# Kernel tuning notes

Hardware: AMD Instinct MI355X
Metric: run time of the kernel (lower is better)

Reference implementation:

```python
import jax, jax.numpy as jnp
import numpy as np

N = 100_000   # total nodes per graph batch
E = 400_000   # directed edges per graph batch
G = 1024      # number of graphs
F_IN = 90


def _lin_init(key, fan_in, fan_out):
    s = 1.0 / np.sqrt(fan_in)
    kW, kb = jax.random.split(key)
    W = jax.random.uniform(kW, (fan_in, fan_out), jnp.float32, -s, s)
    b = jax.random.uniform(kb, (fan_out,), jnp.float32, -s, s)
    return W, b


def setup_inputs() -> dict:
    key = jax.random.key(0)
    ks = jax.random.split(key, 16)
    batch = (jnp.arange(N, dtype=jnp.int32) * G // N).astype(jnp.int32)
    inp = {
        'x1': jax.random.normal(ks[0], (N, F_IN), jnp.float32),
        'edge_index1': jax.random.randint(ks[1], (2, E), 0, N, jnp.int32),
        'batch1': batch,
        'x2': jax.random.normal(ks[2], (N, F_IN), jnp.float32),
        'edge_index2': jax.random.randint(ks[3], (2, E), 0, N, jnp.int32),
        'batch2': batch,
    }
    W1, b1 = _lin_init(ks[4], 90, 128)
    W2, b2 = _lin_init(ks[5], 128, 256)
    W3, b3 = _lin_init(ks[6], 256, 256)
    W4, b4 = _lin_init(ks[7], 256, 256)
    fc1_W, fc1_b = _lin_init(ks[8], 1024, 512)
    fc2_W, fc2_b = _lin_init(ks[9], 512, 256)
    fc3_W, fc3_b = _lin_init(ks[10], 256, 1)
    inp.update(W1=W1, b1=b1, W2=W2, b2=b2, W3=W3, b3=b3, W4=W4, b4=b4,
               fc1_W=fc1_W, fc1_b=fc1_b, fc2_W=fc2_W, fc2_b=fc2_b,
               fc3_W=fc3_W, fc3_b=fc3_b)
    return inp


def _gcn(x, W, b, src, dst, dinv):
    # GCNConv: D^{-1/2} (A + I) D^{-1/2} X W + b  (self-loops added)
    h = x @ W                                   # [N, F_out]
    norm = dinv[src] * dinv[dst]                # [E]
    agg = jax.ops.segment_sum(h[src] * norm[:, None], dst, num_segments=N)
    agg = agg + h * (dinv * dinv)[:, None]      # self-loop term
    return agg + b


def _drug_encoder(x, edge_index, batch, W1, b1, W2, b2, W3, b3, W4, b4):
    src, dst = edge_index[0], edge_index[1]
    # degree with self-loops (PyG gcn_norm)
    deg = jax.ops.segment_sum(jnp.ones(src.shape[0], x.dtype), dst, num_segments=N) + 1.0
    dinv = jax.lax.rsqrt(deg)
    x = jax.nn.relu(_gcn(x, W1, b1, src, dst, dinv))
    x = jax.nn.relu(_gcn(x, W2, b2, src, dst, dinv))
    x = jax.nn.relu(_gcn(x, W3, b3, src, dst, dinv))
    x = jax.nn.relu(_gcn(x, W4, b4, src, dst, dinv))
    gmax = jax.ops.segment_max(x, batch, num_segments=G)
    cnt = jax.ops.segment_sum(jnp.ones(N, x.dtype), batch, num_segments=G)
    gmean = jax.ops.segment_sum(x, batch, num_segments=G) / cnt[:, None]
    return jnp.concatenate([gmax, gmean], axis=1)   # [G, 512]


def reference(x1, edge_index1, batch1, x2, edge_index2, batch2,
              W1, b1, W2, b2, W3, b3, W4, b4,
              fc1_W, fc1_b, fc2_W, fc2_b, fc3_W, fc3_b):
    h1 = _drug_encoder(x1, edge_index1, batch1, W1, b1, W2, b2, W3, b3, W4, b4)
    h2 = _drug_encoder(x2, edge_index2, batch2, W1, b1, W2, b2, W3, b3, W4, b4)
    x = jnp.concatenate([h1 - h2, h2 - h1], axis=1)   # [G, 1024]
    x = jax.nn.relu(x @ fc1_W + fc1_b)                # dropout = identity (eval)
    x = jax.nn.relu(x @ fc2_W + fc2_b)
    x = jnp.tanh(x @ fc3_W + fc3_b)
    return x                                          # [G, 1]
```

## Files before the change

kernel.cpp:

```cpp
#include <hip/hip_runtime.h>
#include <hip/hip_bf16.h>

#define NN 100000
#define EE 400000
#define GG 1024

typedef _Float16 half_t;
typedef _Float16 f16x8 __attribute__((ext_vector_type(8)));
typedef float f32x4 __attribute__((ext_vector_type(4)));

#define GLOAD_LDS(g, l) \
    __builtin_amdgcn_global_load_lds((const __attribute__((address_space(1))) void*)(g), \
                                     (__attribute__((address_space(3))) void*)(l), 16, 0, 0)


__global__ void k_count(const int* __restrict__ ei, int* __restrict__ deg) {
    int e = blockIdx.x * blockDim.x + threadIdx.x;
    if (e < EE) atomicAdd(&deg[ei[EE + e]], 1);
}

__global__ void k_scan_bsum(const int* __restrict__ deg, int* __restrict__ bsum) {
    __shared__ int lds[256];
    int t = threadIdx.x;
    int base = blockIdx.x * 1024 + t * 4;
    int s = 0;
#pragma unroll
    for (int i = 0; i < 4; ++i) { int idx = base + i; s += (idx < NN) ? deg[idx] : 0; }
    lds[t] = s;
    __syncthreads();
    for (int off = 128; off > 0; off >>= 1) {
        if (t < off) lds[t] += lds[t + off];
        __syncthreads();
    }
    if (t == 0) bsum[blockIdx.x] = lds[0];
}

__global__ void k_scan_write(const int* __restrict__ deg, const int* __restrict__ bsum,
                             int* __restrict__ rowptr) {
    __shared__ int lds[256];
    __shared__ int blockoff;
    int t = threadIdx.x;
    if (t == 0) {
        int off = 0;
        for (int b = 0; b < (int)blockIdx.x; ++b) off += bsum[b];
        blockoff = off;
    }
    int base = blockIdx.x * 1024 + t * 4;
    int v[4]; int ts = 0;
#pragma unroll
    for (int i = 0; i < 4; ++i) { int idx = base + i; v[i] = (idx < NN) ? deg[idx] : 0; ts += v[i]; }
    lds[t] = ts;
    __syncthreads();
    for (int off = 1; off < 256; off <<= 1) {
        int x = (t >= off) ? lds[t - off] : 0;
        __syncthreads();
        lds[t] += x;
        __syncthreads();
    }
    int excl = lds[t] - ts + blockoff;
#pragma unroll
    for (int i = 0; i < 4; ++i) {
        int idx = base + i;
        if (idx < NN) rowptr[idx] = excl;
        excl += v[i];
    }
    if (blockIdx.x == 0 && t == 0) rowptr[NN] = EE;
}

__global__ void k_dinv(const int* __restrict__ deg, float* __restrict__ dinv) {
    int i = blockIdx.x * blockDim.x + threadIdx.x;
    if (i < NN) dinv[i] = rsqrtf((float)deg[i] + 1.0f);
}

__global__ void k_fill(const int* __restrict__ ei, const int* __restrict__ rowptr,
                       int* __restrict__ cnt, int* __restrict__ col) {
    int e = blockIdx.x * blockDim.x + threadIdx.x;
    if (e < EE) {
        int s = ei[e], d = ei[EE + e];
        int pos = rowptr[d] + atomicAdd(&cnt[d], 1);
        col[pos] = s;
    }
}


template <int F, int R, int KPAD>
__global__ void k_agg_split(const float* __restrict__ x, const float* __restrict__ dinv,
                            const int* __restrict__ rowptr, const int* __restrict__ col,
                            half_t* __restrict__ out) {
    int wave = threadIdx.x >> 6;
    int lane = threadIdx.x & 63;
    int n = blockIdx.x * 4 + wave;
    if (n >= NN) return;
    float dn = dinv[n];
    const float* xr = x + (size_t)n * F;
    float acc[R];
#pragma unroll
    for (int r = 0; r < R; ++r) {
        int f = lane + 64 * r;
        acc[r] = (f < F) ? dn * xr[f] : 0.f;
    }
    int j0 = rowptr[n], j1 = rowptr[n + 1];
    for (int j = j0; j < j1; ++j) {
        int s = col[j];
        float ds = dinv[s];
        const float* xs = x + (size_t)s * F;
#pragma unroll
        for (int r = 0; r < R; ++r) {
            int f = lane + 64 * r;
            if (f < F) acc[r] += ds * xs[f];
        }
    }
    half_t* o = out + (size_t)n * (2 * KPAD);
#pragma unroll
    for (int r = 0; r < R; ++r) {
        int f = lane + 64 * r;
        if (f < F) {
            float v = dn * acc[r];
            half_t h = (half_t)v;
            half_t l = (half_t)(v - (float)h);
            o[f] = h;
            o[KPAD + f] = l;
        } else if (f < KPAD) {
            o[f] = (half_t)0.f;
            o[KPAD + f] = (half_t)0.f;
        }
    }
}


__global__ void k_wprep(const float* __restrict__ W, half_t* __restrict__ Bt,
                        int K, int Kpad, int Nc) {
    int t = blockIdx.x * 256 + threadIdx.x;
    if (t >= Nc * Kpad) return;
    int n = t / Kpad, kp = t % Kpad;
    half_t h = (half_t)0.f, l = (half_t)0.f;
    if (kp < K) {
        float w = W[(size_t)kp * Nc + n];
        h = (half_t)w;
        l = (half_t)(w - (float)h);
    }
    half_t* o = Bt + (size_t)n * 3 * Kpad;
    o[kp] = h;
    o[Kpad + kp] = h;
    o[2 * Kpad + kp] = l;
}


template <bool RELU>
__global__ __launch_bounds__(256, 2)
void k_mgemm(const half_t* __restrict__ Ap, const half_t* __restrict__ Bt,
             const float* __restrict__ bias, float* __restrict__ C,
             int M, int Kpad, int Nc) {
    __shared__ half_t As[128 * 64];
    __shared__ half_t Bs[128 * 64];
    const int tid = threadIdx.x;
    const int wave = tid >> 6, lane = tid & 63;
    const int wm = wave >> 1, wn = wave & 1;
    const int bm = blockIdx.x * 128, bn = blockIdx.y * 128;
    const int KA = 2 * Kpad, KB = 3 * Kpad;
    const int nkt = KB >> 6;
    const int aTiles = KA >> 6;

    f32x4 acc[4][4] = {};

    const int srow = tid >> 3;
    const int ch = tid & 7;

    for (int kt = 0; kt < nkt; ++kt) {
        int ka0 = ((kt < aTiles) ? kt : (kt - aTiles)) << 6;
        int kb0 = kt << 6;
        __syncthreads();
#pragma unroll
        for (int i = 0; i < 4; ++i) {
            int rl = i * 32 + srow;
            int sch = ch ^ (rl & 7);
            int gr = bm + rl; if (gr >= M) gr = M - 1;
            const half_t* ga = Ap + (size_t)gr * KA + ka0 + sch * 8;
            GLOAD_LDS(ga, (char*)As + i * 4096 + wave * 1024);
        }
#pragma unroll
        for (int i = 0; i < 4; ++i) {
            int rl = i * 32 + srow;
            int sch = ch ^ (rl & 7);
            const half_t* gb = Bt + (size_t)(bn + rl) * KB + kb0 + sch * 8;
            GLOAD_LDS(gb, (char*)Bs + i * 4096 + wave * 1024);
        }
        __syncthreads();
#pragma unroll
        for (int s = 0; s < 2; ++s) {
            f16x8 af[4], bf[4];
#pragma unroll
            for (int i = 0; i < 4; ++i) {
                int row = wm * 64 + i * 16 + (lane & 15);
                int c = s * 4 + (lane >> 4);
                af[i] = *(const f16x8*)&As[row * 64 + ((c ^ (row & 7)) << 3)];
            }
#pragma unroll
            for (int j = 0; j < 4; ++j) {
                int row = wn * 64 + j * 16 + (lane & 15);
                int c = s * 4 + (lane >> 4);
                bf[j] = *(const f16x8*)&Bs[row * 64 + ((c ^ (row & 7)) << 3)];
            }
#pragma unroll
            for (int i = 0; i < 4; ++i)
#pragma unroll
                for (int j = 0; j < 4; ++j)
                    acc[i][j] = __builtin_amdgcn_mfma_f32_16x16x32_f16(af[i], bf[j], acc[i][j], 0, 0, 0);
        }
    }

#pragma unroll
    for (int i = 0; i < 4; ++i) {
#pragma unroll
        for (int j = 0; j < 4; ++j) {
            int cc = bn + wn * 64 + j * 16 + (lane & 15);
            float bv = bias[cc];
            int r0 = bm + wm * 64 + i * 16 + (lane >> 4) * 4;
#pragma unroll
            for (int q = 0; q < 4; ++q) {
                int gr = r0 + q;
                if (gr < M) {
                    float v = acc[i][j][q] + bv;
                    if (RELU) v = fmaxf(v, 0.f);
                    C[(size_t)gr * Nc + cc] = v;
                }
            }
        }
    }
}


template <bool RELU>
__global__ void k_gemm(const float* __restrict__ A, const float* __restrict__ W,
                       const float* __restrict__ bias, float* __restrict__ C,
                       int M, int K, int Nc) {
    __shared__ float As[16][68];
    __shared__ float Bs[16][64];
    int tx = threadIdx.x, ty = threadIdx.y;
    int tid = ty * 16 + tx;
    int bm = blockIdx.x * 64, bn = blockIdx.y * 64;
    float c[4][4] = {};
    int nk = (K + 15) / 16;
    for (int kt = 0; kt < nk; ++kt) {
        int k0 = kt * 16;
        {
            int m = tid >> 2, ks = (tid & 3) * 4;
            int gm = bm + m;
            const float* ap = A + (size_t)gm * K + k0 + ks;
#pragma unroll
            for (int i = 0; i < 4; ++i) {
                int gk = k0 + ks + i;
                As[ks + i][m] = (gm < M && gk < K) ? ap[i] : 0.f;
            }
        }
        {
            int kk = tid >> 4, ns = (tid & 15) * 4;
            int gk = k0 + kk;
            float4 w = make_float4(0.f, 0.f, 0.f, 0.f);
            if (gk < K) w = *(const float4*)(W + (size_t)gk * Nc + bn + ns);
            *(float4*)&Bs[kk][ns] = w;
        }
        __syncthreads();
#pragma unroll
        for (int kk = 0; kk < 16; ++kk) {
            float4 a = *(const float4*)&As[kk][ty * 4];
            float4 b = *(const float4*)&Bs[kk][tx * 4];
            float av[4] = {a.x, a.y, a.z, a.w};
            float bv[4] = {b.x, b.y, b.z, b.w};
#pragma unroll
            for (int i = 0; i < 4; ++i)
#pragma unroll
                for (int j = 0; j < 4; ++j)
                    c[i][j] = fmaf(av[i], bv[j], c[i][j]);
        }
        __syncthreads();
    }
#pragma unroll
    for (int i = 0; i < 4; ++i) {
        int gm = bm + ty * 4 + i;
        if (gm < M) {
            float4 r;
            float* rr = &r.x;
#pragma unroll
            for (int j = 0; j < 4; ++j) {
                float v = c[i][j] + bias[bn + tx * 4 + j];
                if (RELU) v = fmaxf(v, 0.f);
                rr[j] = v;
            }
            *(float4*)(C + (size_t)gm * Nc + bn + tx * 4) = r;
        }
    }
}


__global__ void k_starts(const int* __restrict__ batch, int* __restrict__ gstart) {
    int i = blockIdx.x * blockDim.x + threadIdx.x;
    if (i >= NN) return;
    int b = batch[i];
    if (i == 0) {
        for (int g = 0; g <= b; ++g) gstart[g] = 0;
    } else {
        int pb = batch[i - 1];
        for (int g = pb + 1; g <= b; ++g) gstart[g] = i;
    }
    if (i == NN - 1) {
        for (int g = b + 1; g <= GG; ++g) gstart[g] = NN;
    }
}

__global__ void k_pool(const float* __restrict__ act, const int* __restrict__ gstart,
                       float* __restrict__ h) {
    int g = blockIdx.x;
    int f = threadIdx.x;
    int s = gstart[g], e = gstart[g + 1];
    float mx = 0.f, sm = 0.f;
    for (int i = s; i < e; ++i) {
        float v = act[(size_t)i * 256 + f];
        mx = fmaxf(mx, v);
        sm += v;
    }
    float cnt = (float)(e - s);
    h[(size_t)g * 512 + f] = mx;
    h[(size_t)g * 512 + 256 + f] = (cnt > 0.f) ? sm / cnt : 0.f;
}


__global__ void k_headin(const float* __restrict__ h, float* __restrict__ xh) {
    int t = blockIdx.x * blockDim.x + threadIdx.x;
    if (t >= GG * 1024) return;
    int g = t >> 10, j = t & 1023;
    const float* h1 = h + (size_t)g * 512;
    const float* h2 = h + (size_t)(GG + g) * 512;
    float v = (j < 512) ? (h1[j] - h2[j]) : (h2[j - 512] - h1[j - 512]);
    xh[t] = v;
}

__global__ void k_fc3(const float* __restrict__ A, const float* __restrict__ W,
                      const float* __restrict__ b, float* __restrict__ out) {
    int g = blockIdx.x * 4 + (threadIdx.x >> 6);
    int lane = threadIdx.x & 63;
    const float* a = A + (size_t)g * 256;
    float p = a[lane] * W[lane] + a[lane + 64] * W[lane + 64]
            + a[lane + 128] * W[lane + 128] + a[lane + 192] * W[lane + 192];
    for (int off = 32; off > 0; off >>= 1) p += __shfl_down(p, off);
    if (lane == 0) out[g] = tanhf(p + b[0]);
}


extern "C" void kernel_launch(void* const* d_in, const int* in_sizes, int n_in,
                              void* d_out, int out_size, void* d_ws, size_t ws_size,
                              hipStream_t stream) {
    const float* x1  = (const float*)d_in[0];
    const int*   ei1 = (const int*)d_in[1];
    const int*   ba1 = (const int*)d_in[2];
    const float* x2  = (const float*)d_in[3];
    const int*   ei2 = (const int*)d_in[4];
    const int*   ba2 = (const int*)d_in[5];
    const float* W1 = (const float*)d_in[6];
    const float* b1 = (const float*)d_in[7];
    const float* W2 = (const float*)d_in[8];
    const float* b2 = (const float*)d_in[9];
    const float* W3 = (const float*)d_in[10];
    const float* b3 = (const float*)d_in[11];
    const float* W4 = (const float*)d_in[12];
    const float* b4 = (const float*)d_in[13];
    const float* fc1W = (const float*)d_in[14];
    const float* fc1b = (const float*)d_in[15];
    const float* fc2W = (const float*)d_in[16];
    const float* fc2b = (const float*)d_in[17];
    const float* fc3W = (const float*)d_in[18];
    const float* fc3b = (const float*)d_in[19];
    float* out = (float*)d_out;

    char* ws = (char*)d_ws;
    size_t off = 0;
    auto alloc = [&](size_t bytes) -> void* {
        void* p = (void*)(ws + off);
        off += (bytes + 255) & ~(size_t)255;
        return p;
    };
    int*    deg    = (int*)alloc(NN * sizeof(int));
    int*    rowptr = (int*)alloc((NN + 1) * sizeof(int));
    int*    cnt    = (int*)alloc(NN * sizeof(int));
    int*    col    = (int*)alloc(EE * sizeof(int));
    int*    bsum   = (int*)alloc(128 * sizeof(int));
    int*    gstart = (int*)alloc((GG + 1) * sizeof(int));
    float*  dinv   = (float*)alloc(NN * sizeof(float));
    half_t* Ap     = (half_t*)alloc((size_t)NN * 512 * sizeof(half_t));
    float*  act    = (float*)alloc((size_t)NN * 256 * sizeof(float));
    half_t* Bt1    = (half_t*)alloc((size_t)128 * 384 * sizeof(half_t));
    half_t* Bt2    = (half_t*)alloc((size_t)256 * 384 * sizeof(half_t));
    half_t* Bt3    = (half_t*)alloc((size_t)256 * 768 * sizeof(half_t));
    half_t* Bt4    = (half_t*)alloc((size_t)256 * 768 * sizeof(half_t));
    float*  hpool  = (float*)alloc((size_t)2 * GG * 512 * sizeof(float));
    float*  xh     = (float*)alloc((size_t)GG * 1024 * sizeof(float));
    float*  t1     = (float*)alloc((size_t)GG * 512 * sizeof(float));
    float*  t2     = (float*)alloc((size_t)GG * 256 * sizeof(float));

    dim3 blk(16, 16);
    int nsb = (NN + 1023) / 1024;
    int mt = (NN + 127) / 128;

    k_wprep<<<(128 * 128 + 255) / 256, 256, 0, stream>>>(W1, Bt1, 90, 128, 128);
    k_wprep<<<(256 * 128 + 255) / 256, 256, 0, stream>>>(W2, Bt2, 128, 128, 256);
    k_wprep<<<(256 * 256 + 255) / 256, 256, 0, stream>>>(W3, Bt3, 256, 256, 256);
    k_wprep<<<(256 * 256 + 255) / 256, 256, 0, stream>>>(W4, Bt4, 256, 256, 256);

    for (int p = 0; p < 2; ++p) {
        const float* x   = p ? x2 : x1;
        const int*   ei  = p ? ei2 : ei1;
        const int*   bat = p ? ba2 : ba1;
        hipMemsetAsync(deg, 0, NN * sizeof(int), stream);
        hipMemsetAsync(cnt, 0, NN * sizeof(int), stream);
        k_count<<<(EE + 255) / 256, 256, 0, stream>>>(ei, deg);
        k_scan_bsum<<<nsb, 256, 0, stream>>>(deg, bsum);
        k_scan_write<<<nsb, 256, 0, stream>>>(deg, bsum, rowptr);
        k_dinv<<<(NN + 255) / 256, 256, 0, stream>>>(deg, dinv);
        k_fill<<<(EE + 255) / 256, 256, 0, stream>>>(ei, rowptr, cnt, col);
        k_starts<<<(NN + 255) / 256, 256, 0, stream>>>(bat, gstart);

        k_agg_split<90, 2, 128><<<(NN + 3) / 4, 256, 0, stream>>>(x, dinv, rowptr, col, Ap);
        k_mgemm<true><<<dim3(mt, 1), 256, 0, stream>>>(Ap, Bt1, b1, act, NN, 128, 128);
        k_agg_split<128, 2, 128><<<(NN + 3) / 4, 256, 0, stream>>>(act, dinv, rowptr, col, Ap);
        k_mgemm<true><<<dim3(mt, 2), 256, 0, stream>>>(Ap, Bt2, b2, act, NN, 128, 256);
        k_agg_split<256, 4, 256><<<(NN + 3) / 4, 256, 0, stream>>>(act, dinv, rowptr, col, Ap);
        k_mgemm<true><<<dim3(mt, 2), 256, 0, stream>>>(Ap, Bt3, b3, act, NN, 256, 256);
        k_agg_split<256, 4, 256><<<(NN + 3) / 4, 256, 0, stream>>>(act, dinv, rowptr, col, Ap);
        k_mgemm<true><<<dim3(mt, 2), 256, 0, stream>>>(Ap, Bt4, b4, act, NN, 256, 256);

        k_pool<<<GG, 256, 0, stream>>>(act, gstart, hpool + (size_t)p * GG * 512);
    }

    k_headin<<<(GG * 1024 + 255) / 256, 256, 0, stream>>>(hpool, xh);
    k_gemm<true><<<dim3(GG / 64, 8), blk, 0, stream>>>(xh, fc1W, fc1b, t1, GG, 1024, 512);
    k_gemm<true><<<dim3(GG / 64, 4), blk, 0, stream>>>(t1, fc2W, fc2b, t2, GG, 512, 256);
    k_fc3<<<GG / 4, 256, 0, stream>>>(t2, fc3W, fc3b, out);
}
```

Measured before the change: 1.500 ms.

## Move MLP head GEMMs to split-fp16 MFMA and vectorize hidden aggregation

Replaces the fp32 SIMT GEMMs for fc1 and fc2 with the existing split-fp16 MFMA GEMM. This adds weight prep, hi/lo split kernels for the head inputs, and a split kernel between fc1 and fc2. Hidden-layer aggregation now uses a new vectorized gather kernel that loads 2 or 4 floats per lane instead of the strided per-feature loop. The goal is to cut FMA cost in the head and memory instruction count in aggregation, at the cost of extra small launches and extra traffic to write split buffers.

```diff
diff --git a/kernel.cpp b/kernel.cpp
--- a/kernel.cpp
+++ b/kernel.cpp
@@ -128,6 +128,39 @@
 }
 
 
+template <int VW>
+__global__ void k_agg_splitv(const float* __restrict__ x, const float* __restrict__ dinv,
+                             const int* __restrict__ rowptr, const int* __restrict__ col,
+                             half_t* __restrict__ out) {
+    constexpr int F = 64 * VW;
+    typedef float fvec __attribute__((ext_vector_type(VW)));
+    int wave = threadIdx.x >> 6;
+    int lane = threadIdx.x & 63;
+    int n = blockIdx.x * 4 + wave;
+    if (n >= NN) return;
+    float dn = dinv[n];
+    fvec acc = dn * ((const fvec*)(x + (size_t)n * F))[lane];
+    int j0 = rowptr[n], j1 = rowptr[n + 1];
+    for (int j = j0; j < j1; ++j) {
+        int s = col[j];
+        float ds = dinv[s];
+        acc += ds * ((const fvec*)(x + (size_t)s * F))[lane];
+    }
+    half_t* o = out + (size_t)n * (2 * F);
+    half_t hv[VW], lv[VW];
+#pragma unroll
+    for (int i = 0; i < VW; ++i) {
+        float v = dn * acc[i];
+        hv[i] = (half_t)v;
+        lv[i] = (half_t)(v - (float)hv[i]);
+    }
+#pragma unroll
+    for (int i = 0; i < VW; ++i) o[lane * VW + i] = hv[i];
+#pragma unroll
+    for (int i = 0; i < VW; ++i) o[F + lane * VW + i] = lv[i];
+}
+
+
 __global__ void k_wprep(const float* __restrict__ W, half_t* __restrict__ Bt,
                         int K, int Kpad, int Nc) {
     int t = blockIdx.x * 256 + threadIdx.x;
@@ -143,6 +176,18 @@
     o[kp] = h;
     o[Kpad + kp] = h;
     o[2 * Kpad + kp] = l;
+}
+
+
+__global__ void k_split(const float* __restrict__ in, half_t* __restrict__ out, int K) {
+    int t = blockIdx.x * 256 + threadIdx.x;
+    int row = t / K, k = t % K;
+    float v = in[t];
+    half_t h = (half_t)v;
+    half_t l = (half_t)(v - (float)h);
+    half_t* o = out + (size_t)row * 2 * K;
+    o[k] = h;
+    o[K + k] = l;
 }
 
 
@@ -230,69 +275,6 @@
 }
 
 
-template <bool RELU>
-__global__ void k_gemm(const float* __restrict__ A, const float* __restrict__ W,
-                       const float* __restrict__ bias, float* __restrict__ C,
-                       int M, int K, int Nc) {
-    __shared__ float As[16][68];
-    __shared__ float Bs[16][64];
-    int tx = threadIdx.x, ty = threadIdx.y;
-    int tid = ty * 16 + tx;
-    int bm = blockIdx.x * 64, bn = blockIdx.y * 64;
-    float c[4][4] = {};
-    int nk = (K + 15) / 16;
-    for (int kt = 0; kt < nk; ++kt) {
-        int k0 = kt * 16;
-        {
-            int m = tid >> 2, ks = (tid & 3) * 4;
-            int gm = bm + m;
-            const float* ap = A + (size_t)gm * K + k0 + ks;
-#pragma unroll
-            for (int i = 0; i < 4; ++i) {
-                int gk = k0 + ks + i;
-                As[ks + i][m] = (gm < M && gk < K) ? ap[i] : 0.f;
-            }
-        }
-        {
-            int kk = tid >> 4, ns = (tid & 15) * 4;
-            int gk = k0 + kk;
-            float4 w = make_float4(0.f, 0.f, 0.f, 0.f);
-            if (gk < K) w = *(const float4*)(W + (size_t)gk * Nc + bn + ns);
-            *(float4*)&Bs[kk][ns] = w;
-        }
-        __syncthreads();
-#pragma unroll
-        for (int kk = 0; kk < 16; ++kk) {
-            float4 a = *(const float4*)&As[kk][ty * 4];
-            float4 b = *(const float4*)&Bs[kk][tx * 4];
-            float av[4] = {a.x, a.y, a.z, a.w};
-            float bv[4] = {b.x, b.y, b.z, b.w};
-#pragma unroll
-            for (int i = 0; i < 4; ++i)
-#pragma unroll
-                for (int j = 0; j < 4; ++j)
-                    c[i][j] = fmaf(av[i], bv[j], c[i][j]);
-        }
-        __syncthreads();
-    }
-#pragma unroll
-    for (int i = 0; i < 4; ++i) {
-        int gm = bm + ty * 4 + i;
-        if (gm < M) {
-            float4 r;
-            float* rr = &r.x;
-#pragma unroll
-            for (int j = 0; j < 4; ++j) {
-                float v = c[i][j] + bias[bn + tx * 4 + j];
-                if (RELU) v = fmaxf(v, 0.f);
-                rr[j] = v;
-            }
-            *(float4*)(C + (size_t)gm * Nc + bn + tx * 4) = r;
-        }
-    }
-}
-
-
 __global__ void k_starts(const int* __restrict__ batch, int* __restrict__ gstart) {
     int i = blockIdx.x * blockDim.x + threadIdx.x;
     if (i >= NN) return;
@@ -325,14 +307,18 @@
 }
 
 
-__global__ void k_headin(const float* __restrict__ h, float* __restrict__ xh) {
+__global__ void k_headin_split(const float* __restrict__ h, half_t* __restrict__ xh) {
     int t = blockIdx.x * blockDim.x + threadIdx.x;
     if (t >= GG * 1024) return;
     int g = t >> 10, j = t & 1023;
     const float* h1 = h + (size_t)g * 512;
     const float* h2 = h + (size_t)(GG + g) * 512;
     float v = (j < 512) ? (h1[j] - h2[j]) : (h2[j - 512] - h1[j - 512]);
-    xh[t] = v;
+    half_t hi = (half_t)v;
+    half_t lo = (half_t)(v - (float)hi);
+    half_t* o = xh + (size_t)g * 2048;
+    o[j] = hi;
+    o[1024 + j] = lo;
 }
 
 __global__ void k_fc3(const float* __restrict__ A, const float* __restrict__ W,
@@ -392,12 +378,14 @@
     half_t* Bt2    = (half_t*)alloc((size_t)256 * 384 * sizeof(half_t));
     half_t* Bt3    = (half_t*)alloc((size_t)256 * 768 * sizeof(half_t));
     half_t* Bt4    = (half_t*)alloc((size_t)256 * 768 * sizeof(half_t));
+    half_t* Btf1   = (half_t*)alloc((size_t)512 * 3072 * sizeof(half_t));
+    half_t* Btf2   = (half_t*)alloc((size_t)256 * 1536 * sizeof(half_t));
     float*  hpool  = (float*)alloc((size_t)2 * GG * 512 * sizeof(float));
-    float*  xh     = (float*)alloc((size_t)GG * 1024 * sizeof(float));
+    half_t* xhs    = (half_t*)alloc((size_t)GG * 2048 * sizeof(half_t));
     float*  t1     = (float*)alloc((size_t)GG * 512 * sizeof(float));
+    half_t* t1s    = (half_t*)alloc((size_t)GG * 1024 * sizeof(half_t));
     float*  t2     = (float*)alloc((size_t)GG * 256 * sizeof(float));
 
-    dim3 blk(16, 16);
     int nsb = (NN + 1023) / 1024;
     int mt = (NN + 127) / 128;
 
@@ -405,6 +393,8 @@
     k_wprep<<<(256 * 128 + 255) / 256, 256, 0, stream>>>(W2, Bt2, 128, 128, 256);
     k_wprep<<<(256 * 256 + 255) / 256, 256, 0, stream>>>(W3, Bt3, 256, 256, 256);
     k_wprep<<<(256 * 256 + 255) / 256, 256, 0, stream>>>(W4, Bt4, 256, 256, 256);
+    k_wprep<<<(512 * 1024 + 255) / 256, 256, 0, stream>>>(fc1W, Btf1, 1024, 1024, 512);
+    k_wprep<<<(256 * 512 + 255) / 256, 256, 0, stream>>>(fc2W, Btf2, 512, 512, 256);
 
     for (int p = 0; p < 2; ++p) {
         const float* x   = p ? x2 : x1;
@@ -421,18 +411,19 @@
 
         k_agg_split<90, 2, 128><<<(NN + 3) / 4, 256, 0, stream>>>(x, dinv, rowptr, col, Ap);
         k_mgemm<true><<<dim3(mt, 1), 256, 0, stream>>>(Ap, Bt1, b1, act, NN, 128, 128);
-        k_agg_split<128, 2, 128><<<(NN + 3) / 4, 256, 0, stream>>>(act, dinv, rowptr, col, Ap);
+        k_agg_splitv<2><<<(NN + 3) / 4, 256, 0, stream>>>(act, dinv, rowptr, col, Ap);
         k_mgemm<true><<<dim3(mt, 2), 256, 0, stream>>>(Ap, Bt2, b2, act, NN, 128, 256);
-        k_agg_split<256, 4, 256><<<(NN + 3) / 4, 256, 0, stream>>>(act, dinv, rowptr, col, Ap);
+        k_agg_splitv<4><<<(NN + 3) / 4, 256, 0, stream>>>(act, dinv, rowptr, col, Ap);
         k_mgemm<true><<<dim3(mt, 2), 256, 0, stream>>>(Ap, Bt3, b3, act, NN, 256, 256);
-        k_agg_split<256, 4, 256><<<(NN + 3) / 4, 256, 0, stream>>>(act, dinv, rowptr, col, Ap);
+        k_agg_splitv<4><<<(NN + 3) / 4, 256, 0, stream>>>(act, dinv, rowptr, col, Ap);
         k_mgemm<true><<<dim3(mt, 2), 256, 0, stream>>>(Ap, Bt4, b4, act, NN, 256, 256);
 
         k_pool<<<GG, 256, 0, stream>>>(act, gstart, hpool + (size_t)p * GG * 512);
     }
 
-    k_headin<<<(GG * 1024 + 255) / 256, 256, 0, stream>>>(hpool, xh);
-    k_gemm<true><<<dim3(GG / 64, 8), blk, 0, stream>>>(xh, fc1W, fc1b, t1, GG, 1024, 512);
-    k_gemm<true><<<dim3(GG / 64, 4), blk, 0, stream>>>(t1, fc2W, fc2b, t2, GG, 512, 256);
+    k_headin_split<<<(GG * 1024 + 255) / 256, 256, 0, stream>>>(hpool, xhs);
+    k_mgemm<true><<<dim3(GG / 128, 4), 256, 0, stream>>>(xhs, Btf1, fc1b, t1, GG, 1024, 512);
+    k_split<<<(GG * 512 + 255) / 256, 256, 0, stream>>>(t1, t1s, 512);
+    k_mgemm<true><<<dim3(GG / 128, 2), 256, 0, stream>>>(t1s, Btf2, fc2b, t2, GG, 512, 256);
     k_fc3<<<GG / 4, 256, 0, stream>>>(t2, fc3W, fc3b, out);
 }
```

Result: faster. 1.463 ms (-2.5%).
